# Optimization experiments

Hardware: AMD Instinct MI355X
Metric: run time of the kernel (lower is better)

## Reference

```python
import jax, jax.numpy as jnp
import numpy as np
from functools import reduce

N_QUBITS = 8
DEPTH = 2
DIM = 2 ** N_QUBITS  # state-vector dimension
HIDDEN = 512


def _cnot_chain_np(n):
    # product of CNOT(w, w+1) for w = 0..n-2, wire 0 = most-significant bit (PennyLane order)
    C4 = np.array([[1, 0, 0, 0], [0, 1, 0, 0], [0, 0, 0, 1], [0, 0, 1, 0]], dtype=np.complex64)
    U = np.eye(2 ** n, dtype=np.complex64)
    for w in range(n - 1):
        full = np.kron(np.kron(np.eye(2 ** w, dtype=np.complex64), C4),
                       np.eye(2 ** (n - w - 2), dtype=np.complex64))
        U = full @ U
    return U

CNOT_CHAIN = jnp.asarray(_cnot_chain_np(N_QUBITS))
# PauliZ on wire 0 (MSB): +1 for basis states with MSB=0, -1 otherwise
Z0 = jnp.asarray(np.where(np.arange(DIM) < DIM // 2, 1.0, -1.0).astype(np.float32))


def _rot(p):
    # PennyLane Rot(phi, theta, omega) = RZ(omega) @ RY(theta) @ RZ(phi)
    phi, th, om = p[0], p[1], p[2]
    c = jnp.cos(th / 2).astype(jnp.complex64)
    s = jnp.sin(th / 2).astype(jnp.complex64)
    ep = jnp.exp(-0.5j * (phi + om).astype(jnp.complex64))  # e^{-i(phi+om)/2}
    em = jnp.exp(0.5j * (phi - om).astype(jnp.complex64))   # e^{ i(phi-om)/2}
    m00 = ep * c
    m01 = -em * s
    m10 = jnp.conj(em) * s
    m11 = jnp.conj(ep) * c
    return jnp.stack([jnp.stack([m00, m01]), jnp.stack([m10, m11])])


def _gate_unitary(P):
    # P: (depth, n_qubits, 3). Circuit (after data RX): per layer Rot on every wire, then CNOT chain.
    U = jnp.eye(DIM, dtype=jnp.complex64)
    for l in range(DEPTH):
        layer = reduce(jnp.kron, [_rot(P[l, w]) for w in range(N_QUBITS)])
        U = CNOT_CHAIN @ (layer @ U)
    return U


def _expval(theta, U):
    # RX(theta)|0...0> = cos(t/2)|0..0> - i sin(t/2)|10..0>; then fixed unitary U; <Z_0>
    col0 = U[:, 0]          # U |00...0>
    col1 = U[:, DIM // 2]   # U |10...0>
    a = jnp.cos(theta / 2)[:, None]
    b = jnp.sin(theta / 2)[:, None]
    psi = a * col0[None, :] - 1j * b * col1[None, :]  # (B, DIM)
    return jnp.sum(Z0 * (psi.real ** 2 + psi.imag ** 2), axis=-1)  # (B,)


def setup_inputs() -> dict:
    key = jax.random.key(0)
    ks = jax.random.split(key, 13)
    T, B, D, H, Q = 256, 128, 512, HIDDEN, N_QUBITS
    inp = {"inputs": jax.random.normal(ks[0], (T, B, D), jnp.float32)}
    for i, g in enumerate(["f", "i", "g", "o"]):
        inp[f"W{g}"] = jax.random.normal(ks[1 + 3 * i], (Q, D + H), jnp.float32) * 0.02
        inp[f"b{g}"] = jnp.zeros((Q,), jnp.float32)
        inp[f"P{g}"] = jax.random.normal(ks[3 + 3 * i], (DEPTH, Q, 3), jnp.float32)
    return inp


def reference(inputs, Wf, bf, Pf, Wi, bi, Pi, Wg, bg, Pg, Wo, bo, Po):
    Uf, Ui, Ug, Uo = _gate_unitary(Pf), _gate_unitary(Pi), _gate_unitary(Pg), _gate_unitary(Po)

    def step(carry, x):
        hx, cx = carry
        comb = jnp.concatenate([x, hx], axis=1)  # (B, D+H)
        f = jax.nn.sigmoid(_expval((comb @ Wf.T + bf)[:, 0], Uf))[:, None]
        i = jax.nn.sigmoid(_expval((comb @ Wi.T + bi)[:, 0], Ui))[:, None]
        g = jnp.tanh(_expval((comb @ Wg.T + bg)[:, 0], Ug))[:, None]
        o = jax.nn.sigmoid(_expval((comb @ Wo.T + bo)[:, 0], Uo))[:, None]
        cx = f * cx + i * g
        hx = o * jnp.tanh(cx)
        return (hx, cx), hx

    B = inputs.shape[1]
    init = (jnp.zeros((B, HIDDEN), inputs.dtype), jnp.zeros((B, HIDDEN), inputs.dtype))
    (hx, cx), outputs = jax.lax.scan(step, init, inputs)
    return outputs, hx, cx
```

## Files before the change

### kernel.cpp

```cpp
#include <hip/hip_runtime.h>
#include <math.h>

#define T_STEPS 256
#define BATCH   128
#define DIMD    512
#define NROWS   (T_STEPS * BATCH)
#define PF      16
#define WRITER_BLOCKS 258

#define INV2PI  0.15915494309189535f
#define L2E     1.4426950408889634f
#define TWO_L2E 2.8853900817779268f

#define AGENT __HIP_MEMORY_SCOPE_AGENT

#if __has_builtin(__builtin_amdgcn_sinf)
#define HW_SIN(x) __builtin_amdgcn_sinf(x)
#else
__device__ __forceinline__ float HW_SIN(float x) { return __sinf(x * 6.283185307179586f); }
#endif
#if __has_builtin(__builtin_amdgcn_exp2f)
#define EXP2(x) __builtin_amdgcn_exp2f(x)
#else
#define EXP2(x) exp2f(x)
#endif
#if __has_builtin(__builtin_amdgcn_rcpf)
#define RCP(x) __builtin_amdgcn_rcpf(x)
#else
#define RCP(x) (1.0f / (x))
#endif

__device__ __forceinline__ void  st_rlx(float* p, float v) {
    __hip_atomic_store(p, v, __ATOMIC_RELAXED, AGENT);
}
__device__ __forceinline__ void  st_rlx_i(int* p, int v) {
    __hip_atomic_store(p, v, __ATOMIC_RELAXED, AGENT);
}
__device__ __forceinline__ int   ld_rlx_i(const int* p) {
    return __hip_atomic_load(p, __ATOMIC_RELAXED, AGENT);
}
#define VMFENCE() asm volatile("s_waitcnt vmcnt(0)" ::: "memory")
#define CFENCE()  asm volatile("" ::: "memory")

__global__ __launch_bounds__(256) void qconsts(
    const float* __restrict__ Pf, const float* __restrict__ Pi,
    const float* __restrict__ Pg, const float* __restrict__ Po,
    const float* __restrict__ Wf, const float* __restrict__ Wi,
    const float* __restrict__ Wg, const float* __restrict__ Wo,
    float* __restrict__ gc, int* __restrict__ hProg)
{
    const int g    = threadIdx.x >> 6;
    const int lane = threadIdx.x & 63;
    if (threadIdx.x == 0) { hProg[0] = 0; hProg[1] = 0; }
    const float* P = (g == 0) ? Pf : (g == 1) ? Pi : (g == 2) ? Pg : Po;
    const float* W = (g == 0) ? Wf : (g == 1) ? Wi : (g == 2) ? Wg : Wo;

    __shared__ float s0r[4][256], s0i[4][256], s1r[4][256], s1i[4][256];

#pragma unroll
    for (int j = 0; j < 4; ++j) {
        const int k = lane + 64 * j;
        s0r[g][k] = (k == 0)   ? 1.0f : 0.0f;  s0i[g][k] = 0.0f;
        s1r[g][k] = (k == 128) ? 1.0f : 0.0f;  s1i[g][k] = 0.0f;
    }
    __syncthreads();

    for (int l = 0; l < 2; ++l) {
        for (int w = 0; w < 8; ++w) {
            const float phi = P[l * 24 + w * 3 + 0];
            const float th  = P[l * 24 + w * 3 + 1];
            const float om  = P[l * 24 + w * 3 + 2];
            float sh, chh; __sincosf(0.5f * th, &sh, &chh);
            float sp, cp;  __sincosf(0.5f * (phi + om), &sp, &cp);
            float sm, cm;  __sincosf(0.5f * (phi - om), &sm, &cm);
            const float m00r =  cp * chh, m00i = -sp * chh;
            const float m01r = -cm * sh,  m01i = -sm * sh;
            const float m10r =  cm * sh,  m10i = -sm * sh;
            const float m11r =  cp * chh, m11i =  sp * chh;

            const int shift = 7 - w;
            const int mask  = 1 << shift;

            float n0r[4], n0i[4], n1r[4], n1i[4];
#pragma unroll
            for (int j = 0; j < 4; ++j) {
                const int k  = lane + 64 * j;
                const int bit = (k >> shift) & 1;
                const int i0 = k & ~mask, i1 = k | mask;
                const float a0r = s0r[g][i0], a0i = s0i[g][i0];
                const float a1r = s0r[g][i1], a1i = s0i[g][i1];
                const float b0r = s1r[g][i0], b0i = s1i[g][i0];
                const float b1r = s1r[g][i1], b1i = s1i[g][i1];
                const float mr0 = bit ? m10r : m00r, mi0 = bit ? m10i : m00i;
                const float mr1 = bit ? m11r : m01r, mi1 = bit ? m11i : m01i;
                n0r[j] = mr0 * a0r - mi0 * a0i + mr1 * a1r - mi1 * a1i;
                n0i[j] = mr0 * a0i + mi0 * a0r + mr1 * a1i + mi1 * a1r;
                n1r[j] = mr0 * b0r - mi0 * b0i + mr1 * b1r - mi1 * b1i;
                n1i[j] = mr0 * b0i + mi0 * b0r + mr1 * b1i + mi1 * b1r;
            }
            __syncthreads();
#pragma unroll
            for (int j = 0; j < 4; ++j) {
                const int k = lane + 64 * j;
                s0r[g][k] = n0r[j]; s0i[g][k] = n0i[j];
                s1r[g][k] = n1r[j]; s1i[g][k] = n1i[j];
            }
            __syncthreads();
        }
        float n0r[4], n0i[4], n1r[4], n1i[4];
#pragma unroll
        for (int j = 0; j < 4; ++j) {
            int src = lane + 64 * j;
            for (int w = 6; w >= 0; --w) {
                const int cb = (src >> (7 - w)) & 1;
                src ^= cb << (6 - w);
            }
            n0r[j] = s0r[g][src]; n0i[j] = s0i[g][src];
            n1r[j] = s1r[g][src]; n1i[j] = s1i[g][src];
        }
        __syncthreads();
#pragma unroll
        for (int j = 0; j < 4; ++j) {
            const int k = lane + 64 * j;
            s0r[g][k] = n0r[j]; s0i[g][k] = n0i[j];
            s1r[g][k] = n1r[j]; s1i[g][k] = n1i[j];
        }
        __syncthreads();
    }

    float t00 = 0, t11 = 0, t01 = 0;
#pragma unroll
    for (int j = 0; j < 4; ++j) {
        const int k = lane + 64 * j;
        const float z = (k < 128) ? 1.0f : -1.0f;
        t00 += z * (s0r[g][k] * s0r[g][k] + s0i[g][k] * s0i[g][k]);
        t11 += z * (s1r[g][k] * s1r[g][k] + s1i[g][k] * s1i[g][k]);
        t01 += z * (s0i[g][k] * s1r[g][k] - s0r[g][k] * s1i[g][k]);
    }
    float tsw = 0;
#pragma unroll
    for (int j = 0; j < 8; ++j) tsw += W[512 + lane + 64 * j];

    for (int off = 32; off; off >>= 1) {
        t00 += __shfl_xor(t00, off);
        t11 += __shfl_xor(t11, off);
        t01 += __shfl_xor(t01, off);
        tsw += __shfl_xor(tsw, off);
    }
    if (lane == 0) {
        const float A  = 0.5f * (t00 + t11);
        const float Bc = 0.5f * (t00 - t11);
        const float Bs = -t01;
        const float R  = sqrtf(Bc * Bc + Bs * Bs);
        const float ph = atan2f(Bc, Bs) * INV2PI;
        const float sc = (g == 2) ? TWO_L2E : -L2E;
        gc[4 * g + 0] = sc * A;
        gc[4 * g + 1] = sc * R;
        gc[4 * g + 2] = ph;
        gc[4 * g + 3] = tsw * INV2PI;
    }
}

__global__ __launch_bounds__(256) void gemv4(
    const float* __restrict__ x,
    const float* __restrict__ Wf, const float* __restrict__ Wi,
    const float* __restrict__ Wg, const float* __restrict__ Wo,
    const float* __restrict__ bfp, const float* __restrict__ bip,
    const float* __restrict__ bgp, const float* __restrict__ bop,
    const float* __restrict__ gc,
    float4* __restrict__ X4)
{
    const int lane = threadIdx.x & 63;
    const int wid  = threadIdx.x >> 6;
    const int row  = (blockIdx.x << 2) + wid;

    const float4* xr = (const float4*)(x + (size_t)row * DIMD);
    const float4 xa = xr[lane];
    const float4 xb = xr[lane + 64];

    const float4* wfp = (const float4*)Wf;
    const float4* wip = (const float4*)Wi;
    const float4* wgp = (const float4*)Wg;
    const float4* wop = (const float4*)Wo;
    const float4 fa = wfp[lane], fb = wfp[lane + 64];
    const float4 ia = wip[lane], ib = wip[lane + 64];
    const float4 ga = wgp[lane], gb = wgp[lane + 64];
    const float4 oa = wop[lane], ob = wop[lane + 64];

    float sf = xa.x * fa.x + xa.y * fa.y + xa.z * fa.z + xa.w * fa.w
             + xb.x * fb.x + xb.y * fb.y + xb.z * fb.z + xb.w * fb.w;
    float si = xa.x * ia.x + xa.y * ia.y + xa.z * ia.z + xa.w * ia.w
             + xb.x * ib.x + xb.y * ib.y + xb.z * ib.z + xb.w * ib.w;
    float sg = xa.x * ga.x + xa.y * ga.y + xa.z * ga.z + xa.w * ga.w
             + xb.x * gb.x + xb.y * gb.y + xb.z * gb.z + xb.w * gb.w;
    float so = xa.x * oa.x + xa.y * oa.y + xa.z * oa.z + xa.w * oa.w
             + xb.x * ob.x + xb.y * ob.y + xb.z * ob.z + xb.w * ob.w;

    for (int off = 32; off; off >>= 1) {
        sf += __shfl_xor(sf, off);
        si += __shfl_xor(si, off);
        sg += __shfl_xor(sg, off);
        so += __shfl_xor(so, off);
    }
    if (lane == 0) {
        X4[row] = make_float4(fmaf(sf + bfp[0], INV2PI, gc[2]),
                              fmaf(si + bip[0], INV2PI, gc[6]),
                              fmaf(sg + bgp[0], INV2PI, gc[10]),
                              fmaf(so + bop[0], INV2PI, gc[14]));
    }
}

__global__ __launch_bounds__(256) void scan_write(
    const float4* __restrict__ X4, const float* __restrict__ gc,
    float* __restrict__ Hs, float* __restrict__ cfin,
    float4* __restrict__ out4, int* __restrict__ hProg)
{
    const int bid  = blockIdx.x;
    const int wv   = threadIdx.x >> 6;
    const int lane = threadIdx.x & 63;

    if (bid == 0) {
        if (threadIdx.x >= BATCH) return;
        const int b = threadIdx.x;

        const float Af = gc[0],  Rf = gc[1],  swf = gc[3];
        const float Ai = gc[4],  Ri = gc[5],  swi = gc[7];
        const float Ag = gc[8],  Rg = gc[9],  swg = gc[11];
        const float Ao = gc[12], Ro = gc[13], swo = gc[15];

        float4 p[PF];
#pragma unroll
        for (int j = 0; j < PF; ++j) p[j] = X4[j * BATCH + b];

        float c = 0.0f, h = 0.0f;
        for (int tb = 0; tb < T_STEPS; tb += PF) {
#pragma unroll
            for (int j = 0; j < PF; ++j) {
                const int t = tb + j;
                const float4 xv = p[j];
                p[j] = X4[(t + PF) * BATCH + b];

                const float thf = fmaf(h, swf, xv.x);
                const float thi = fmaf(h, swi, xv.y);
                const float thg = fmaf(h, swg, xv.z);
                const float tho = fmaf(h, swo, xv.w);
                const float Ef = fmaf(Rf, HW_SIN(thf), Af);
                const float Ei = fmaf(Ri, HW_SIN(thi), Ai);
                const float Eg = fmaf(Rg, HW_SIN(thg), Ag);
                const float Eo = fmaf(Ro, HW_SIN(tho), Ao);
                const float fg = RCP(1.0f + EXP2(Ef));
                const float ig = RCP(1.0f + EXP2(Ei));
                const float og = RCP(1.0f + EXP2(Eo));
                const float gg = 1.0f - 2.0f * RCP(EXP2(Eg) + 1.0f);
                c = fmaf(fg, c, ig * gg);
                const float y = RCP(EXP2(c * TWO_L2E) + 1.0f);
                h = fmaf(-2.0f * og, y, og);
                st_rlx(&Hs[t * BATCH + b], h);
            }
            if (tb == T_STEPS - PF) st_rlx(&cfin[b], c);
            if (((tb + PF) & 31) == 0) {
                VMFENCE();
                if (lane == 0) st_rlx_i(&hProg[wv], tb + PF);
            }
        }
        return;
    }

    const int t  = bid - 1;
    const int qd = wv;
    const int pidx = (qd < 2) ? 0 : 1;
    const int need = (t < 256) ? (t + 1) : 256;

    int cur = ld_rlx_i(&hProg[pidx]);
    while (cur < need) {
        int chunks = ((need - cur) >> 4) + 1;
        for (int s = 0; s < chunks; ++s) __builtin_amdgcn_s_sleep(16);
        cur = ld_rlx_i(&hProg[pidx]);
    }
    CFENCE();

    const float* src = (t == 257) ? cfin : (Hs + ((t >= 256 ? 255 : t) * BATCH));
    const float hv = src[qd * 32 + (lane & 31)];

    size_t base = (t < 256) ? ((size_t)t * 16384)
                : (t == 256 ? (size_t)4194304 : (size_t)4210688);
    base += (size_t)qd * 4096;
#pragma unroll 8
    for (int j = 0; j < 64; ++j) {
        const float v = __shfl(hv, j >> 1);
        out4[base + j * 64 + lane] = make_float4(v, v, v, v);
    }
}

extern "C" void kernel_launch(void* const* d_in, const int* in_sizes, int n_in,
                              void* d_out, int out_size, void* d_ws, size_t ws_size,
                              hipStream_t stream)
{
    const float* inp = (const float*)d_in[0];
    const float* Wf  = (const float*)d_in[1];
    const float* bfv = (const float*)d_in[2];
    const float* Pf  = (const float*)d_in[3];
    const float* Wi  = (const float*)d_in[4];
    const float* biv = (const float*)d_in[5];
    const float* Pi  = (const float*)d_in[6];
    const float* Wg  = (const float*)d_in[7];
    const float* bgv = (const float*)d_in[8];
    const float* Pg  = (const float*)d_in[9];
    const float* Wo  = (const float*)d_in[10];
    const float* bov = (const float*)d_in[11];
    const float* Po  = (const float*)d_in[12];

    float4* X4   = (float4*)d_ws;
    float*  Hs   = (float*)(X4 + NROWS + PF * BATCH);
    float*  cfin = Hs + NROWS;
    float*  gc   = cfin + BATCH;
    int*    hProg = (int*)(gc + 16);

    qconsts<<<1, 256, 0, stream>>>(Pf, Pi, Pg, Po, Wf, Wi, Wg, Wo, gc, hProg);
    gemv4<<<NROWS / 4, 256, 0, stream>>>(inp, Wf, Wi, Wg, Wo,
                                         bfv, biv, bgv, bov, gc, X4);
    scan_write<<<1 + WRITER_BLOCKS, 256, 0, stream>>>(X4, gc, Hs, cfin,
                                                      (float4*)d_out, hProg);
}
```

Baseline: 66.10 us.

## Fuse quantum-constant and input GEMV kernels into one launch, four rows per wave

```diff
diff --git a/kernel.cpp b/kernel.cpp
--- a/kernel.cpp
+++ b/kernel.cpp
@@ -7,6 +7,7 @@
 #define NROWS   (T_STEPS * BATCH)
 #define PF      16
 #define WRITER_BLOCKS 258
+#define GEMV_BLOCKS 2048
 
 #define INV2PI  0.15915494309189535f
 #define L2E     1.4426950408889634f
@@ -42,61 +43,89 @@
 #define VMFENCE() asm volatile("s_waitcnt vmcnt(0)" ::: "memory")
 #define CFENCE()  asm volatile("" ::: "memory")
 
-__global__ __launch_bounds__(256) void qconsts(
+__global__ __launch_bounds__(256) void prep(
+    const float* __restrict__ inp,
+    const float* __restrict__ Wf, const float* __restrict__ Wi,
+    const float* __restrict__ Wg, const float* __restrict__ Wo,
+    const float* __restrict__ bfp, const float* __restrict__ bip,
+    const float* __restrict__ bgp, const float* __restrict__ bop,
     const float* __restrict__ Pf, const float* __restrict__ Pi,
     const float* __restrict__ Pg, const float* __restrict__ Po,
-    const float* __restrict__ Wf, const float* __restrict__ Wi,
-    const float* __restrict__ Wg, const float* __restrict__ Wo,
-    float* __restrict__ gc, int* __restrict__ hProg)
+    float* __restrict__ gc, int* __restrict__ hProg,
+    float4* __restrict__ X4)
 {
-    const int g    = threadIdx.x >> 6;
+    const int bid  = blockIdx.x;
+    const int wv   = threadIdx.x >> 6;
     const int lane = threadIdx.x & 63;
-    if (threadIdx.x == 0) { hProg[0] = 0; hProg[1] = 0; }
-    const float* P = (g == 0) ? Pf : (g == 1) ? Pi : (g == 2) ? Pg : Po;
-    const float* W = (g == 0) ? Wf : (g == 1) ? Wi : (g == 2) ? Wg : Wo;
-
-    __shared__ float s0r[4][256], s0i[4][256], s1r[4][256], s1i[4][256];
-
-#pragma unroll
-    for (int j = 0; j < 4; ++j) {
-        const int k = lane + 64 * j;
-        s0r[g][k] = (k == 0)   ? 1.0f : 0.0f;  s0i[g][k] = 0.0f;
-        s1r[g][k] = (k == 128) ? 1.0f : 0.0f;  s1i[g][k] = 0.0f;
-    }
-    __syncthreads();
-
-    for (int l = 0; l < 2; ++l) {
-        for (int w = 0; w < 8; ++w) {
-            const float phi = P[l * 24 + w * 3 + 0];
-            const float th  = P[l * 24 + w * 3 + 1];
-            const float om  = P[l * 24 + w * 3 + 2];
-            float sh, chh; __sincosf(0.5f * th, &sh, &chh);
-            float sp, cp;  __sincosf(0.5f * (phi + om), &sp, &cp);
-            float sm, cm;  __sincosf(0.5f * (phi - om), &sm, &cm);
-            const float m00r =  cp * chh, m00i = -sp * chh;
-            const float m01r = -cm * sh,  m01i = -sm * sh;
-            const float m10r =  cm * sh,  m10i = -sm * sh;
-            const float m11r =  cp * chh, m11i =  sp * chh;
-
-            const int shift = 7 - w;
-            const int mask  = 1 << shift;
-
+
+    if (bid == 0) {
+        if (threadIdx.x == 0) { hProg[0] = 0; hProg[1] = 0; }
+        const int g = wv;
+        const float* P = (g == 0) ? Pf : (g == 1) ? Pi : (g == 2) ? Pg : Po;
+        const float* W = (g == 0) ? Wf : (g == 1) ? Wi : (g == 2) ? Wg : Wo;
+
+        __shared__ float s0r[4][256], s0i[4][256], s1r[4][256], s1i[4][256];
+
+#pragma unroll
+        for (int j = 0; j < 4; ++j) {
+            const int k = lane + 64 * j;
+            s0r[g][k] = (k == 0)   ? 1.0f : 0.0f;  s0i[g][k] = 0.0f;
+            s1r[g][k] = (k == 128) ? 1.0f : 0.0f;  s1i[g][k] = 0.0f;
+        }
+        __syncthreads();
+
+        for (int l = 0; l < 2; ++l) {
+            for (int w = 0; w < 8; ++w) {
+                const float phi = P[l * 24 + w * 3 + 0];
+                const float th  = P[l * 24 + w * 3 + 1];
+                const float om  = P[l * 24 + w * 3 + 2];
+                float sh, chh; __sincosf(0.5f * th, &sh, &chh);
+                float sp, cp;  __sincosf(0.5f * (phi + om), &sp, &cp);
+                float sm, cm;  __sincosf(0.5f * (phi - om), &sm, &cm);
+                const float m00r =  cp * chh, m00i = -sp * chh;
+                const float m01r = -cm * sh,  m01i = -sm * sh;
+                const float m10r =  cm * sh,  m10i = -sm * sh;
+                const float m11r =  cp * chh, m11i =  sp * chh;
+
+                const int shift = 7 - w;
+                const int mask  = 1 << shift;
+
+                float n0r[4], n0i[4], n1r[4], n1i[4];
+#pragma unroll
+                for (int j = 0; j < 4; ++j) {
+                    const int k  = lane + 64 * j;
+                    const int bit = (k >> shift) & 1;
+                    const int i0 = k & ~mask, i1 = k | mask;
+                    const float a0r = s0r[g][i0], a0i = s0i[g][i0];
+                    const float a1r = s0r[g][i1], a1i = s0i[g][i1];
+                    const float b0r = s1r[g][i0], b0i = s1i[g][i0];
+                    const float b1r = s1r[g][i1], b1i = s1i[g][i1];
+                    const float mr0 = bit ? m10r : m00r, mi0 = bit ? m10i : m00i;
+                    const float mr1 = bit ? m11r : m01r, mi1 = bit ? m11i : m01i;
+                    n0r[j] = mr0 * a0r - mi0 * a0i + mr1 * a1r - mi1 * a1i;
+                    n0i[j] = mr0 * a0i + mi0 * a0r + mr1 * a1i + mi1 * a1r;
+                    n1r[j] = mr0 * b0r - mi0 * b0i + mr1 * b1r - mi1 * b1i;
+                    n1i[j] = mr0 * b0i + mi0 * b0r + mr1 * b1i + mi1 * b1r;
+                }
+                __syncthreads();
+#pragma unroll
+                for (int j = 0; j < 4; ++j) {
+                    const int k = lane + 64 * j;
+                    s0r[g][k] = n0r[j]; s0i[g][k] = n0i[j];
+                    s1r[g][k] = n1r[j]; s1i[g][k] = n1i[j];
+                }
+                __syncthreads();
+            }
             float n0r[4], n0i[4], n1r[4], n1i[4];
 #pragma unroll
             for (int j = 0; j < 4; ++j) {
-                const int k  = lane + 64 * j;
-                const int bit = (k >> shift) & 1;
-                const int i0 = k & ~mask, i1 = k | mask;
-                const float a0r = s0r[g][i0], a0i = s0i[g][i0];
-                const float a1r = s0r[g][i1], a1i = s0i[g][i1];
-                const float b0r = s1r[g][i0], b0i = s1i[g][i0];
-                const float b1r = s1r[g][i1], b1i = s1i[g][i1];
-                const float mr0 = bit ? m10r : m00r, mi0 = bit ? m10i : m00i;
-                const float mr1 = bit ? m11r : m01r, mi1 = bit ? m11i : m01i;
-                n0r[j] = mr0 * a0r - mi0 * a0i + mr1 * a1r - mi1 * a1i;
-                n0i[j] = mr0 * a0i + mi0 * a0r + mr1 * a1i + mi1 * a1r;
-                n1r[j] = mr0 * b0r - mi0 * b0i + mr1 * b1r - mi1 * b1i;
-                n1i[j] = mr0 * b0i + mi0 * b0r + mr1 * b1i + mi1 * b1r;
+                int src = lane + 64 * j;
+                for (int w = 6; w >= 0; --w) {
+                    const int cb = (src >> (7 - w)) & 1;
+                    src ^= cb << (6 - w);
+                }
+                n0r[j] = s0r[g][src]; n0i[j] = s0i[g][src];
+                n1r[j] = s1r[g][src]; n1i[j] = s1i[g][src];
             }
             __syncthreads();
 #pragma unroll
@@ -107,76 +136,42 @@
             }
             __syncthreads();
         }
-        float n0r[4], n0i[4], n1r[4], n1i[4];
-#pragma unroll
-        for (int j = 0; j < 4; ++j) {
-            int src = lane + 64 * j;
-            for (int w = 6; w >= 0; --w) {
-                const int cb = (src >> (7 - w)) & 1;
-                src ^= cb << (6 - w);
-            }
-            n0r[j] = s0r[g][src]; n0i[j] = s0i[g][src];
-            n1r[j] = s1r[g][src]; n1i[j] = s1i[g][src];
-        }
-        __syncthreads();
+
+        float t00 = 0, t11 = 0, t01 = 0;
 #pragma unroll
         for (int j = 0; j < 4; ++j) {
             const int k = lane + 64 * j;
-            s0r[g][k] = n0r[j]; s0i[g][k] = n0i[j];
-            s1r[g][k] = n1r[j]; s1i[g][k] = n1i[j];
-        }
-        __syncthreads();
-    }
-
-    float t00 = 0, t11 = 0, t01 = 0;
-#pragma unroll
-    for (int j = 0; j < 4; ++j) {
-        const int k = lane + 64 * j;
-        const float z = (k < 128) ? 1.0f : -1.0f;
-        t00 += z * (s0r[g][k] * s0r[g][k] + s0i[g][k] * s0i[g][k]);
-        t11 += z * (s1r[g][k] * s1r[g][k] + s1i[g][k] * s1i[g][k]);
-        t01 += z * (s0i[g][k] * s1r[g][k] - s0r[g][k] * s1i[g][k]);
-    }
-    float tsw = 0;
-#pragma unroll
-    for (int j = 0; j < 8; ++j) tsw += W[512 + lane + 64 * j];
-
-    for (int off = 32; off; off >>= 1) {
-        t00 += __shfl_xor(t00, off);
-        t11 += __shfl_xor(t11, off);
-        t01 += __shfl_xor(t01, off);
-        tsw += __shfl_xor(tsw, off);
-    }
-    if (lane == 0) {
-        const float A  = 0.5f * (t00 + t11);
-        const float Bc = 0.5f * (t00 - t11);
-        const float Bs = -t01;
-        const float R  = sqrtf(Bc * Bc + Bs * Bs);
-        const float ph = atan2f(Bc, Bs) * INV2PI;
-        const float sc = (g == 2) ? TWO_L2E : -L2E;
-        gc[4 * g + 0] = sc * A;
-        gc[4 * g + 1] = sc * R;
-        gc[4 * g + 2] = ph;
-        gc[4 * g + 3] = tsw * INV2PI;
-    }
-}
-
-__global__ __launch_bounds__(256) void gemv4(
-    const float* __restrict__ x,
-    const float* __restrict__ Wf, const float* __restrict__ Wi,
-    const float* __restrict__ Wg, const float* __restrict__ Wo,
-    const float* __restrict__ bfp, const float* __restrict__ bip,
-    const float* __restrict__ bgp, const float* __restrict__ bop,
-    const float* __restrict__ gc,
-    float4* __restrict__ X4)
-{
-    const int lane = threadIdx.x & 63;
-    const int wid  = threadIdx.x >> 6;
-    const int row  = (blockIdx.x << 2) + wid;
-
-    const float4* xr = (const float4*)(x + (size_t)row * DIMD);
-    const float4 xa = xr[lane];
-    const float4 xb = xr[lane + 64];
+            const float z = (k < 128) ? 1.0f : -1.0f;
+            t00 += z * (s0r[g][k] * s0r[g][k] + s0i[g][k] * s0i[g][k]);
+            t11 += z * (s1r[g][k] * s1r[g][k] + s1i[g][k] * s1i[g][k]);
+            t01 += z * (s0i[g][k] * s1r[g][k] - s0r[g][k] * s1i[g][k]);
+        }
+        float tsw = 0;
+#pragma unroll
+        for (int j = 0; j < 8; ++j) tsw += W[512 + lane + 64 * j];
+
+        for (int off = 32; off; off >>= 1) {
+            t00 += __shfl_xor(t00, off);
+            t11 += __shfl_xor(t11, off);
+            t01 += __shfl_xor(t01, off);
+            tsw += __shfl_xor(tsw, off);
+        }
+        if (lane == 0) {
+            const float A  = 0.5f * (t00 + t11);
+            const float Bc = 0.5f * (t00 - t11);
+            const float Bs = -t01;
+            const float R  = sqrtf(Bc * Bc + Bs * Bs);
+            const float ph = atan2f(Bc, Bs) * INV2PI;
+            const float sc = (g == 2) ? TWO_L2E : -L2E;
+            gc[4 * g + 0] = sc * A;
+            gc[4 * g + 1] = sc * R;
+            gc[4 * g + 2] = ph;
+            gc[4 * g + 3] = tsw * INV2PI;
+        }
+        return;
+    }
+
+    const int rowbase = (bid - 1) * 16 + wv * 4;
 
     const float4* wfp = (const float4*)Wf;
     const float4* wip = (const float4*)Wi;
@@ -187,26 +182,37 @@
     const float4 ga = wgp[lane], gb = wgp[lane + 64];
     const float4 oa = wop[lane], ob = wop[lane + 64];
 
-    float sf = xa.x * fa.x + xa.y * fa.y + xa.z * fa.z + xa.w * fa.w
-             + xb.x * fb.x + xb.y * fb.y + xb.z * fb.z + xb.w * fb.w;
-    float si = xa.x * ia.x + xa.y * ia.y + xa.z * ia.z + xa.w * ia.w
-             + xb.x * ib.x + xb.y * ib.y + xb.z * ib.z + xb.w * ib.w;
-    float sg = xa.x * ga.x + xa.y * ga.y + xa.z * ga.z + xa.w * ga.w
-             + xb.x * gb.x + xb.y * gb.y + xb.z * gb.z + xb.w * gb.w;
-    float so = xa.x * oa.x + xa.y * oa.y + xa.z * oa.z + xa.w * oa.w
-             + xb.x * ob.x + xb.y * ob.y + xb.z * ob.z + xb.w * ob.w;
-
-    for (int off = 32; off; off >>= 1) {
-        sf += __shfl_xor(sf, off);
-        si += __shfl_xor(si, off);
-        sg += __shfl_xor(sg, off);
-        so += __shfl_xor(so, off);
-    }
+    const float4* xr = (const float4*)(inp + (size_t)rowbase * DIMD);
+    float sums[4][4];
+#pragma unroll
+    for (int r = 0; r < 4; ++r) {
+        const float4 xa = xr[r * 128 + lane];
+        const float4 xb = xr[r * 128 + lane + 64];
+        sums[r][0] = xa.x * fa.x + xa.y * fa.y + xa.z * fa.z + xa.w * fa.w
+                   + xb.x * fb.x + xb.y * fb.y + xb.z * fb.z + xb.w * fb.w;
+        sums[r][1] = xa.x * ia.x + xa.y * ia.y + xa.z * ia.z + xa.w * ia.w
+                   + xb.x * ib.x + xb.y * ib.y + xb.z * ib.z + xb.w * ib.w;
+        sums[r][2] = xa.x * ga.x + xa.y * ga.y + xa.z * ga.z + xa.w * ga.w
+                   + xb.x * gb.x + xb.y * gb.y + xb.z * gb.z + xb.w * gb.w;
+        sums[r][3] = xa.x * oa.x + xa.y * oa.y + xa.z * oa.z + xa.w * oa.w
+                   + xb.x * ob.x + xb.y * ob.y + xb.z * ob.z + xb.w * ob.w;
+    }
+#pragma unroll
+    for (int r = 0; r < 4; ++r)
+#pragma unroll
+        for (int g = 0; g < 4; ++g)
+            for (int off = 32; off; off >>= 1)
+                sums[r][g] += __shfl_xor(sums[r][g], off);
+
     if (lane == 0) {
-        X4[row] = make_float4(fmaf(sf + bfp[0], INV2PI, gc[2]),
-                              fmaf(si + bip[0], INV2PI, gc[6]),
-                              fmaf(sg + bgp[0], INV2PI, gc[10]),
-                              fmaf(so + bop[0], INV2PI, gc[14]));
+        const float b0f = bfp[0], b0i = bip[0], b0g = bgp[0], b0o = bop[0];
+#pragma unroll
+        for (int r = 0; r < 4; ++r) {
+            X4[rowbase + r] = make_float4((sums[r][0] + b0f) * INV2PI,
+                                          (sums[r][1] + b0i) * INV2PI,
+                                          (sums[r][2] + b0g) * INV2PI,
+                                          (sums[r][3] + b0o) * INV2PI);
+        }
     }
 }
 
@@ -223,10 +229,10 @@
         if (threadIdx.x >= BATCH) return;
         const int b = threadIdx.x;
 
-        const float Af = gc[0],  Rf = gc[1],  swf = gc[3];
-        const float Ai = gc[4],  Ri = gc[5],  swi = gc[7];
-        const float Ag = gc[8],  Rg = gc[9],  swg = gc[11];
-        const float Ao = gc[12], Ro = gc[13], swo = gc[15];
+        const float Af = gc[0],  Rf = gc[1],  phf = gc[2],  swf = gc[3];
+        const float Ai = gc[4],  Ri = gc[5],  phi_ = gc[6], swi = gc[7];
+        const float Ag = gc[8],  Rg = gc[9],  phg = gc[10], swg = gc[11];
+        const float Ao = gc[12], Ro = gc[13], pho = gc[14], swo = gc[15];
 
         float4 p[PF];
 #pragma unroll
@@ -240,10 +246,10 @@
                 const float4 xv = p[j];
                 p[j] = X4[(t + PF) * BATCH + b];
 
-                const float thf = fmaf(h, swf, xv.x);
-                const float thi = fmaf(h, swi, xv.y);
-                const float thg = fmaf(h, swg, xv.z);
-                const float tho = fmaf(h, swo, xv.w);
+                const float thf = fmaf(h, swf, xv.x + phf);
+                const float thi = fmaf(h, swi, xv.y + phi_);
+                const float thg = fmaf(h, swg, xv.z + phg);
+                const float tho = fmaf(h, swo, xv.w + pho);
                 const float Ef = fmaf(Rf, HW_SIN(thf), Af);
                 const float Ei = fmaf(Ri, HW_SIN(thi), Ai);
                 const float Eg = fmaf(Rg, HW_SIN(thg), Ag);
@@ -316,9 +322,10 @@
     float*  gc   = cfin + BATCH;
     int*    hProg = (int*)(gc + 16);
 
-    qconsts<<<1, 256, 0, stream>>>(Pf, Pi, Pg, Po, Wf, Wi, Wg, Wo, gc, hProg);
-    gemv4<<<NROWS / 4, 256, 0, stream>>>(inp, Wf, Wi, Wg, Wo,
-                                         bfv, biv, bgv, bov, gc, X4);
+    prep<<<1 + GEMV_BLOCKS, 256, 0, stream>>>(inp, Wf, Wi, Wg, Wo,
+                                              bfv, biv, bgv, bov,
+                                              Pf, Pi, Pg, Po,
+                                              gc, hProg, X4);
     scan_write<<<1 + WRITER_BLOCKS, 256, 0, stream>>>(X4, gc, Hs, cfin,
                                                       (float4*)d_out, hProg);
 }
```

Result: faster. 57.17 us (-13.5%).
